# Performance work log

Measured on AMD Instinct MI355X. Metric: run time of the kernel, lower is better.

## Reference

```python
import jax, jax.numpy as jnp
import numpy as np

MAX_LEN_SEQ = 2048
MAX_LEN_PAD = 2176
MIN_LEN_SEG = 32
MAX_LEN_SEG = 128
S = MAX_LEN_SEQ // MIN_LEN_SEG + 1  # max_num_seg = 65
B = 16
D = 128
R = B * S          # 1040 segment rows
W = 2 * MAX_LEN_SEG  # 256 candidate positions per segment


def _forward(x, scales, len_seq, len_seg_raw):
    T = x.shape[1]
    sc = scales + 0.5                                   # (R,) in [0.5, 1.5)
    idx = jnp.arange(W, dtype=jnp.float32)              # (W,)
    idx_scaled = idx[None, :] / sc[:, None]             # (R, W)
    idx_fl = jnp.floor(idx_scaled)
    lam = idx_scaled - idx_fl                           # (R, W)
    len_seg = (len_seg_raw.astype(jnp.int32) + MIN_LEN_SEG)  # (R, 1)
    mask1 = idx_fl < (len_seg.astype(jnp.float32) - 1.0)
    # per-batch cumulative segment offsets
    offset = jnp.cumsum(len_seg.reshape(B, S), axis=-1)
    offset = jnp.pad(offset[:, :-1], ((0, 0), (1, 0))).reshape(R, 1)
    idx_org = idx_fl + offset.astype(jnp.float32)       # (R, W) source positions
    len_rp = jnp.repeat(len_seq.astype(jnp.float32), S)  # (R,)
    mask2 = idx_org < (len_rp - 1.0)[:, None]
    mask = (mask1 & mask2).reshape(-1)                  # (R*W,) row-major like boolean_mask

    pos = jnp.cumsum(mask.astype(jnp.int32)) - 1        # compacted slot for masked entries
    total = jnp.sum(mask.astype(jnp.int32))

    bidx = jnp.broadcast_to((jnp.arange(R) // S)[:, None], (R, W)).reshape(-1)
    i_fl = jnp.clip(idx_org.astype(jnp.int32).reshape(-1), 0, T - 1)
    i_cl = jnp.clip(i_fl + 1, 0, T - 1)
    y_fl = x[bidx, i_fl]                                # (R*W, D)
    y_cl = x[bidx, i_cl]
    lamf = lam.reshape(-1)[:, None]
    y = (1.0 - lamf) * y_fl + lamf * y_cl               # (R*W, D)

    # compact masked rows into dense buffer (extra row N swallows unmasked)
    N = R * W
    buf = jnp.zeros((N + 1, D), x.dtype)
    buf = buf.at[jnp.where(mask, pos, N)].set(y)

    # emulate y[: total//B*B].reshape(B, -1, D)[:, :MAX_LEN_SEQ] + pad
    L = total // B
    t = jnp.arange(MAX_LEN_SEQ)
    gidx = jnp.arange(B)[:, None] * L + t[None, :]      # (B, MAX_LEN_SEQ)
    out = buf[jnp.clip(gidx, 0, N)]
    out = jnp.where((t < L)[None, :, None], out, jnp.zeros((), x.dtype))
    return out


def setup_inputs() -> dict:
    key = jax.random.key(0)
    k1, k2, k3, k4 = jax.random.split(key, 4)
    x = jax.random.normal(k1, (B, MAX_LEN_PAD, D), dtype=jnp.float32)
    scales = jax.random.uniform(k2, (R,), dtype=jnp.float32)
    len_seq = jax.random.randint(k3, (B,), MAX_LEN_SEQ // 2, MAX_LEN_SEQ, dtype=jnp.int32)
    len_seq = len_seq.at[0].set(MAX_LEN_SEQ)  # force max(len_seq) == MAX_LEN_SEQ (static)
    len_seg_raw = jax.random.randint(k4, (R, 1), 0, MAX_LEN_SEG - MIN_LEN_SEG, dtype=jnp.int32)
    return {"x": x, "scales": scales, "len_seq": len_seq, "len_seg_raw": len_seg_raw}


def reference(x, scales, len_seq, len_seg_raw):
    return _forward(x, scales, len_seq, len_seg_raw)
```

## Files before the change

### kernel.cpp

```cpp
#include <hip/hip_runtime.h>

#define B_      16
#define S_      65
#define R_      1040
#define W_      256
#define T_      2176
#define D_      128
#define MAXSEQ  2048

__global__ __launch_bounds__(256) void interp_setup(
    const float* __restrict__ scales,
    const int*   __restrict__ len_seq,
    const int*   __restrict__ len_seg_raw,
    int* __restrict__ lut,
    int* __restrict__ meta)
{
    __shared__ int s_len[R_];
    __shared__ int s_off[R_];
    __shared__ int s_wtot[4];
    const int tid  = threadIdx.x;
    const int lane = tid & 63;
    const int wid  = tid >> 6;

    for (int r = tid; r < R_; r += 256) s_len[r] = len_seg_raw[r] + 32;
    __syncthreads();

    for (int b = wid; b < B_; b += 4) {
        int v = s_len[b * S_ + lane];
        int incl = v;
        #pragma unroll
        for (int d = 1; d < 64; d <<= 1) {
            int n = __shfl_up(incl, d, 64);
            if (lane >= d) incl += n;
        }
        s_off[b * S_ + lane] = incl - v;
        int tot = __shfl(incl, 63, 64);
        if (lane == 0) s_off[b * S_ + 64] = tot;
    }
    __syncthreads();

    int c[5], off5[5];
    const int r0 = tid * 5;
    int tsum = 0;
    #pragma unroll
    for (int i = 0; i < 5; ++i) {
        int r = r0 + i, cc = 0, off = 0;
        if (r < R_) {
            float sc = scales[r] + 0.5f;
            off = s_off[r];
            int K = min(s_len[r] - 1, len_seq[r / S_] - 1 - off);
            if (K > 0) {
                cc = (int)ceilf((float)K * sc);
                cc = min(max(cc, 0), W_);
                const float Kf = (float)K;
                while (cc > 0  && ((float)(cc - 1) / sc) >= Kf) --cc;
                while (cc < W_ && ((float)cc       / sc) <  Kf) ++cc;
            }
        }
        c[i] = cc; off5[i] = off; tsum += cc;
    }

    int incl = tsum;
    #pragma unroll
    for (int d = 1; d < 64; d <<= 1) {
        int n = __shfl_up(incl, d, 64);
        if (lane >= d) incl += n;
    }
    if (lane == 63) s_wtot[wid] = incl;
    __syncthreads();
    int wpre = 0, total = 0;
    #pragma unroll
    for (int wv = 0; wv < 4; ++wv) {
        int t_ = s_wtot[wv];
        if (wv < wid) wpre += t_;
        total += t_;
    }
    int base = wpre + incl - tsum;

    #pragma unroll
    for (int i = 0; i < 5; ++i) {
        int r = r0 + i;
        if (r < R_) {
            int tag = (off5[i] << 19) | (r << 8);
            for (int w = 0; w < c[i]; ++w) lut[base + w] = tag | w;
            base += c[i];
        }
    }
    if (tid == 0) { meta[0] = total; meta[1] = total / B_; }
}

__global__ __launch_bounds__(256) void interp_gather(
    const float* __restrict__ x,
    const float* __restrict__ scales,
    const int*   __restrict__ lut,
    const int*   __restrict__ meta,
    float* __restrict__ out)
{
    __shared__ int s_L;
    if (threadIdx.x == 0) s_L = meta[1];
    __syncthreads();
    const int L = s_L;

    const int tid  = threadIdx.x;
    const int orow = blockIdx.x * 8 + (tid >> 5);
    const int lane = tid & 31;
    float4* outp = (float4*)(out + (size_t)orow * D_) + lane;

    const int t = orow & (MAXSEQ - 1);
    const int b = orow >> 11;
    if (t >= L) { *outp = make_float4(0.f, 0.f, 0.f, 0.f); return; }

    const int v   = lut[b * L + t];
    const int w   = v & 255;
    const int r   = (v >> 8) & 2047;
    const int off = v >> 19;

    const float sc  = scales[r] + 0.5f;
    const float is  = (float)w / sc;
    const float fl  = floorf(is);
    const float lam = is - fl;
    const int i0 = (int)fl + off;
    const int bs = r / S_;

    const float* base = x + (size_t)bs * (T_ * D_);
    const float4* pa = (const float4*)(base + (size_t)i0 * D_) + lane;
    const float4* pb = (const float4*)(base + (size_t)(i0 + 1) * D_) + lane;
    const float4 a = *pa, cc = *pb;
    const float om = 1.0f - lam;
    float4 y;
    y.x = om * a.x + lam * cc.x;
    y.y = om * a.y + lam * cc.y;
    y.z = om * a.z + lam * cc.z;
    y.w = om * a.w + lam * cc.w;
    *outp = y;
}

extern "C" void kernel_launch(void* const* d_in, const int* in_sizes, int n_in,
                              void* d_out, int out_size, void* d_ws, size_t ws_size,
                              hipStream_t stream) {
    const float* x           = (const float*)d_in[0];
    const float* scales      = (const float*)d_in[1];
    const int*   len_seq     = (const int*)d_in[2];
    const int*   len_seg_raw = (const int*)d_in[3];
    float*       out         = (float*)d_out;

    int* lut  = (int*)d_ws;
    int* meta = lut + R_ * W_;

    interp_setup<<<1, 256, 0, stream>>>(scales, len_seq, len_seg_raw, lut, meta);

    const int nrows = B_ * MAXSEQ;
    interp_gather<<<nrows / 8, 256, 0, stream>>>(x, scales, lut, meta, out);
}
```

Baseline: 100.8 us.

## Replace per-element lookup table with row-start prefix array and binary search

The single-block setup kernel no longer writes a packed tag for every compacted output position. It now stores only per-segment source offsets and exclusive prefix starts. The gather kernel loads these arrays into shared memory and binary-searches the segment for each output row. This removes the serial per-thread LUT fill in the one-block setup kernel, at the cost of a shared-memory preload and a log-depth search in every gather block.

New measurement: 87.27 us. 1.15x faster.

```diff
diff --git a/kernel.cpp b/kernel.cpp
--- a/kernel.cpp
+++ b/kernel.cpp
@@ -12,7 +12,8 @@
     const float* __restrict__ scales,
     const int*   __restrict__ len_seq,
     const int*   __restrict__ len_seg_raw,
-    int* __restrict__ lut,
+    int* __restrict__ offs,
+    int* __restrict__ row_start,
     int* __restrict__ meta)
 {
     __shared__ int s_len[R_];
@@ -39,15 +40,15 @@
     }
     __syncthreads();
 
-    int c[5], off5[5];
+    int c[5];
     const int r0 = tid * 5;
     int tsum = 0;
     #pragma unroll
     for (int i = 0; i < 5; ++i) {
-        int r = r0 + i, cc = 0, off = 0;
+        int r = r0 + i, cc = 0;
         if (r < R_) {
             float sc = scales[r] + 0.5f;
-            off = s_off[r];
+            int off = s_off[r];
             int K = min(s_len[r] - 1, len_seq[r / S_] - 1 - off);
             if (K > 0) {
                 cc = (int)ceilf((float)K * sc);
@@ -56,8 +57,9 @@
                 while (cc > 0  && ((float)(cc - 1) / sc) >= Kf) --cc;
                 while (cc < W_ && ((float)cc       / sc) <  Kf) ++cc;
             }
+            offs[r] = off;
         }
-        c[i] = cc; off5[i] = off; tsum += cc;
+        c[i] = cc; tsum += cc;
     }
 
     int incl = tsum;
@@ -80,28 +82,31 @@
     #pragma unroll
     for (int i = 0; i < 5; ++i) {
         int r = r0 + i;
-        if (r < R_) {
-            int tag = (off5[i] << 19) | (r << 8);
-            for (int w = 0; w < c[i]; ++w) lut[base + w] = tag | w;
-            base += c[i];
-        }
+        if (r < R_) { row_start[r] = base; base += c[i]; }
     }
-    if (tid == 0) { meta[0] = total; meta[1] = total / B_; }
+    if (tid == 0) {
+        row_start[R_] = total;
+        meta[0] = total;
+        meta[1] = total / B_;
+    }
 }
 
 __global__ __launch_bounds__(256) void interp_gather(
     const float* __restrict__ x,
     const float* __restrict__ scales,
-    const int*   __restrict__ lut,
+    const int*   __restrict__ offs,
+    const int*   __restrict__ row_start,
     const int*   __restrict__ meta,
     float* __restrict__ out)
 {
-    __shared__ int s_L;
-    if (threadIdx.x == 0) s_L = meta[1];
+    __shared__ int s_rs[R_ + 1];
+    __shared__ int s_of[R_];
+    const int tid = threadIdx.x;
+    for (int i = tid; i < R_ + 1; i += 256) s_rs[i] = row_start[i];
+    for (int i = tid; i < R_;     i += 256) s_of[i] = offs[i];
     __syncthreads();
-    const int L = s_L;
 
-    const int tid  = threadIdx.x;
+    const int L    = meta[1];
     const int orow = blockIdx.x * 8 + (tid >> 5);
     const int lane = tid & 31;
     float4* outp = (float4*)(out + (size_t)orow * D_) + lane;
@@ -110,16 +115,20 @@
     const int b = orow >> 11;
     if (t >= L) { *outp = make_float4(0.f, 0.f, 0.f, 0.f); return; }
 
-    const int v   = lut[b * L + t];
-    const int w   = v & 255;
-    const int r   = (v >> 8) & 2047;
-    const int off = v >> 19;
+    const int g = b * L + t;
+    int lo = 0, hi = R_;
+    while (hi - lo > 1) {
+        int mid = (lo + hi) >> 1;
+        if (s_rs[mid] <= g) lo = mid; else hi = mid;
+    }
+    const int r = lo;
+    const int w = g - s_rs[r];
 
     const float sc  = scales[r] + 0.5f;
     const float is  = (float)w / sc;
     const float fl  = floorf(is);
     const float lam = is - fl;
-    const int i0 = (int)fl + off;
+    const int i0 = (int)fl + s_of[r];
     const int bs = r / S_;
 
     const float* base = x + (size_t)bs * (T_ * D_);
@@ -144,11 +153,14 @@
     const int*   len_seg_raw = (const int*)d_in[3];
     float*       out         = (float*)d_out;
 
-    int* lut  = (int*)d_ws;
-    int* meta = lut + R_ * W_;
+    int* offs      = (int*)d_ws;
+    int* row_start = offs + R_;
+    int* meta      = row_start + R_ + 1;
 
-    interp_setup<<<1, 256, 0, stream>>>(scales, len_seq, len_seg_raw, lut, meta);
+    interp_setup<<<1, 256, 0, stream>>>(scales, len_seq, len_seg_raw,
+                                        offs, row_start, meta);
 
     const int nrows = B_ * MAXSEQ;
-    interp_gather<<<nrows / 8, 256, 0, stream>>>(x, scales, lut, meta, out);
+    interp_gather<<<nrows / 8, 256, 0, stream>>>(x, scales, offs, row_start,
+                                                 meta, out);
 }
```
